# Performance work log

Measured on AMD Instinct MI355X. Metric: run time of the kernel, lower is better.

## Reference

```python
import jax, jax.numpy as jnp
import numpy as np

N_PTS = 32768      # n_x == n_y (query points == source points)
K_NBR = 32         # neighbors per query point
N_EDGES = N_PTS * K_NBR
D_COORD = 3
C = 64             # f_y channels == MLP output channels
H = 256            # MLP hidden width


def setup_inputs() -> dict:
    key = jax.random.key(0)
    ks = jax.random.split(key, 12)
    y = jax.random.normal(ks[0], (N_PTS, D_COORD), dtype=jnp.float32)
    x = jax.random.normal(ks[1], (N_PTS, D_COORD), dtype=jnp.float32)
    f_y = jax.random.normal(ks[2], (N_PTS, C), dtype=jnp.float32)
    neighbors_index = jax.random.randint(ks[3], (N_EDGES,), 0, N_PTS, dtype=jnp.int64)
    neighbors_row_splits = (jnp.arange(N_PTS + 1, dtype=jnp.int64) * K_NBR)
    weights = jax.random.uniform(ks[4], (N_EDGES,), dtype=jnp.float32)
    # LinearChannelMLP params: layers [6, 256, 256, 64], gelu between layers
    def dense(k, fan_in, fan_out):
        w = jax.random.normal(k, (fan_in, fan_out), dtype=jnp.float32) / np.sqrt(fan_in)
        return w
    W0 = dense(ks[5], 2 * D_COORD, H)
    b0 = jnp.zeros((H,), dtype=jnp.float32)
    W1 = dense(ks[6], H, H)
    b1 = jnp.zeros((H,), dtype=jnp.float32)
    W2 = dense(ks[7], H, C)
    b2 = jnp.zeros((C,), dtype=jnp.float32)
    return {"y": y, "x": x, "f_y": f_y,
            "neighbors_index": neighbors_index,
            "neighbors_row_splits": neighbors_row_splits,
            "weights": weights,
            "W0": W0, "b0": b0, "W1": W1, "b1": b1, "W2": W2, "b2": b2}


def reference(y, x, f_y, neighbors_index, neighbors_row_splits, weights,
              W0, b0, W1, b1, W2, b2):
    n_x = neighbors_row_splits.shape[0] - 1
    n_edges = neighbors_index.shape[0]
    # CSR row id for each edge (equivalent to repeat(arange(n_x), num_reps))
    seg = jnp.searchsorted(neighbors_row_splits, jnp.arange(n_edges), side='right') - 1
    rep_features = y[neighbors_index]            # [E, 3] gathered source coords
    self_features = x[seg]                       # [E, 3] repeated query coords
    agg = jnp.concatenate([rep_features, self_features], axis=-1)  # [E, 6]
    # channel MLP (gelu between layers, none after last)
    h = jax.nn.gelu(agg @ W0 + b0)
    h = jax.nn.gelu(h @ W1 + b1)
    rep = h @ W2 + b2                            # [E, C] kernel values
    # transform_type='linear': kernel * f_y(neighbor)
    rep = rep * f_y[neighbors_index]
    # quadrature weights (forces sum reduction, as in source)
    rep = rep * weights[:, None]
    out = jax.ops.segment_sum(rep, seg, num_segments=n_x)  # segment-CSR sum
    return out
```

## Files before the change

kernel.cpp:

```cpp
#include <hip/hip_runtime.h>
#include <hip/hip_bf16.h>
#include <stdint.h>

#define NPTS 32768
#define KNBR 32
#define NEDGES (NPTS * KNBR)
#define TM 128
#define AGG_STRIDE 40
#define H_STRIDE 264

typedef __attribute__((ext_vector_type(8))) short short8;
typedef __attribute__((ext_vector_type(4))) float f32x4;
typedef __attribute__((ext_vector_type(4))) unsigned int u32x4;

__device__ __forceinline__ unsigned short f2bf(float f) {
    unsigned int u = __float_as_uint(f);
    unsigned int r = (u + 0x7FFFu + ((u >> 16) & 1u)) >> 16;
    return (unsigned short)r;
}

__device__ __forceinline__ float gelu_tanh(float x) {
    float x2 = x * x;
    float inner = x * fmaf(0.044715f, x2, 1.0f);
    float e = __builtin_amdgcn_exp2f(-2.30220824f * inner);
    return x * __builtin_amdgcn_rcpf(1.0f + e);
}

__global__ void pack_w(const float* __restrict__ W0, const float* __restrict__ W1,
                       const float* __restrict__ W2, unsigned short* __restrict__ wp) {
    int tid = blockIdx.x * blockDim.x + threadIdx.x;
    if (tid >= 11264) return;
    unsigned short v[8];
    int l = tid & 63;
    if (tid < 1024) {
        int nt = tid >> 6;
        int n = nt * 16 + (l & 15);
        int k0 = (l >> 4) << 3;
        #pragma unroll
        for (int j = 0; j < 8; ++j) {
            int k = k0 + j;
            v[j] = f2bf(k < 6 ? W0[k * 256 + n] : 0.0f);
        }
    } else if (tid < 9216) {
        int q = tid - 1024;
        int nt = (q >> 6) & 15;
        int s = q >> 10;
        int n = nt * 16 + (l & 15);
        int k0 = s * 32 + ((l >> 4) << 3);
        #pragma unroll
        for (int j = 0; j < 8; ++j) v[j] = f2bf(W1[(k0 + j) * 256 + n]);
    } else {
        int q = tid - 9216;
        int nt = (q >> 6) & 3;
        int s = q >> 8;
        int n = nt * 16 + (l & 15);
        int k0 = s * 32 + ((l >> 4) << 3);
        #pragma unroll
        for (int j = 0; j < 8; ++j) v[j] = f2bf(W2[(k0 + j) * 64 + n]);
    }
    unsigned short* o = &wp[tid * 8];
    #pragma unroll
    for (int j = 0; j < 8; ++j) o[j] = v[j];
}

__global__ __launch_bounds__(256, 2)
void gno_fused(const float* __restrict__ y, const float* __restrict__ x,
               const float* __restrict__ f_y, const int* __restrict__ nbr,
               const float* __restrict__ wts,
               const float* __restrict__ b0, const float* __restrict__ b1,
               const float* __restrict__ b2,
               const unsigned short* __restrict__ wp,
               float* __restrict__ out) {
    __shared__ unsigned short agg_lds[TM * AGG_STRIDE];
    __shared__ unsigned short h_lds[TM * H_STRIDE];

    const int b = blockIdx.x;
    const int tid = threadIdx.x;
    const int l = tid & 63;
    const int w = tid >> 6;
    const int lg = l >> 4;
    const int ln = l & 15;
    const int ebase = b * TM;

    if (tid < TM) {
        int e = ebase + tid;
        int j = nbr[e];
        int i = e >> 5;
        float a0 = y[j * 3 + 0], a1 = y[j * 3 + 1], a2 = y[j * 3 + 2];
        float a3 = x[i * 3 + 0], a4 = x[i * 3 + 1], a5 = x[i * 3 + 2];
        unsigned int p0 = (unsigned int)f2bf(a0) | ((unsigned int)f2bf(a1) << 16);
        unsigned int p1 = (unsigned int)f2bf(a2) | ((unsigned int)f2bf(a3) << 16);
        unsigned int p2 = (unsigned int)f2bf(a4) | ((unsigned int)f2bf(a5) << 16);
        u32x4 q0 = {p0, p1, p2, 0u};
        u32x4 z  = {0u, 0u, 0u, 0u};
        unsigned short* row = &agg_lds[tid * AGG_STRIDE];
        *(u32x4*)(row +  0) = q0;
        *(u32x4*)(row +  8) = z;
        *(u32x4*)(row + 16) = z;
        *(u32x4*)(row + 24) = z;
    }
    __syncthreads();

    {
        short8 bw[4];
        float b0v[4];
        #pragma unroll
        for (int n = 0; n < 4; ++n) {
            int nt = 4 * w + n;
            bw[n] = *(const short8*)&wp[(nt * 64 + l) * 8];
            b0v[n] = b0[nt * 16 + ln];
        }
        f32x4 zero = {0.f, 0.f, 0.f, 0.f};
        #pragma unroll
        for (int mt = 0; mt < 8; ++mt) {
            short8 a = *(const short8*)&agg_lds[(mt * 16 + ln) * AGG_STRIDE + lg * 8];
            #pragma unroll
            for (int n = 0; n < 4; ++n) {
                f32x4 c = __builtin_amdgcn_mfma_f32_16x16x32_bf16(a, bw[n], zero, 0, 0, 0);
                int col = (4 * w + n) * 16 + ln;
                #pragma unroll
                for (int i = 0; i < 4; ++i) {
                    float g = gelu_tanh(c[i] + b0v[n]);
                    h_lds[(mt * 16 + lg * 4 + i) * H_STRIDE + col] = f2bf(g);
                }
            }
        }
    }
    __syncthreads();

    f32x4 acc[8][4];
    #pragma unroll
    for (int mt = 0; mt < 8; ++mt)
        #pragma unroll
        for (int n = 0; n < 4; ++n)
            acc[mt][n] = (f32x4){0.f, 0.f, 0.f, 0.f};

    for (int s = 0; s < 8; ++s) {
        short8 bw[4];
        #pragma unroll
        for (int n = 0; n < 4; ++n)
            bw[n] = *(const short8*)&wp[(1024 + (s * 16 + 4 * w + n) * 64 + l) * 8];
        #pragma unroll
        for (int mt = 0; mt < 8; ++mt) {
            short8 a = *(const short8*)&h_lds[(mt * 16 + ln) * H_STRIDE + s * 32 + lg * 8];
            #pragma unroll
            for (int n = 0; n < 4; ++n)
                acc[mt][n] = __builtin_amdgcn_mfma_f32_16x16x32_bf16(a, bw[n], acc[mt][n], 0, 0, 0);
        }
    }
    __syncthreads();

    {
        float b1v[4];
        #pragma unroll
        for (int n = 0; n < 4; ++n) b1v[n] = b1[(4 * w + n) * 16 + ln];
        #pragma unroll
        for (int mt = 0; mt < 8; ++mt) {
            #pragma unroll
            for (int n = 0; n < 4; ++n) {
                int col = (4 * w + n) * 16 + ln;
                #pragma unroll
                for (int i = 0; i < 4; ++i) {
                    float g = gelu_tanh(acc[mt][n][i] + b1v[n]);
                    h_lds[(mt * 16 + lg * 4 + i) * H_STRIDE + col] = f2bf(g);
                }
            }
        }
    }
    __syncthreads();

    f32x4 acc3[8];
    #pragma unroll
    for (int mt = 0; mt < 8; ++mt) acc3[mt] = (f32x4){0.f, 0.f, 0.f, 0.f};

    for (int s = 0; s < 8; ++s) {
        short8 bw = *(const short8*)&wp[(9216 + (s * 4 + w) * 64 + l) * 8];
        #pragma unroll
        for (int mt = 0; mt < 8; ++mt) {
            short8 a = *(const short8*)&h_lds[(mt * 16 + ln) * H_STRIDE + s * 32 + lg * 8];
            acc3[mt] = __builtin_amdgcn_mfma_f32_16x16x32_bf16(a, bw, acc3[mt], 0, 0, 0);
        }
    }

    {
        int col = w * 16 + ln;
        float b2v = b2[col];
        float p[4] = {0.f, 0.f, 0.f, 0.f};
        #pragma unroll
        for (int mt = 0; mt < 8; ++mt) {
            #pragma unroll
            for (int i = 0; i < 4; ++i) {
                int el = mt * 16 + lg * 4 + i;
                int e = ebase + el;
                int j = nbr[e];
                float v = acc3[mt][i] + b2v;
                v *= f_y[j * 64 + col] * wts[e];
                p[mt >> 1] += v;
            }
        }
        #pragma unroll
        for (int g = 0; g < 4; ++g) {
            float v = p[g];
            v += __shfl_xor(v, 16, 64);
            v += __shfl_xor(v, 32, 64);
            if (lg == 0) out[(b * 4 + g) * 64 + col] = v;
        }
    }
}

extern "C" void kernel_launch(void* const* d_in, const int* in_sizes, int n_in,
                              void* d_out, int out_size, void* d_ws, size_t ws_size,
                              hipStream_t stream) {
    const float* y   = (const float*)d_in[0];
    const float* x   = (const float*)d_in[1];
    const float* f_y = (const float*)d_in[2];
    const int*   nbr = (const int*)d_in[3];
    const float* wts = (const float*)d_in[5];
    const float* W0  = (const float*)d_in[6];
    const float* b0  = (const float*)d_in[7];
    const float* W1  = (const float*)d_in[8];
    const float* b1  = (const float*)d_in[9];
    const float* W2  = (const float*)d_in[10];
    const float* b2  = (const float*)d_in[11];
    unsigned short* wp = (unsigned short*)d_ws;
    float* out = (float*)d_out;

    pack_w<<<dim3(44), dim3(256), 0, stream>>>(W0, W1, W2, wp);
    gno_fused<<<dim3(NEDGES / TM), dim3(256), 0, stream>>>(
        y, x, f_y, nbr, wts, b0, b1, b2, wp, out);
}
```

Baseline: 304.4 us.

## Transpose MFMA operands, halve edge tile, vectorize LDS stores and epilogue

Swaps the MFMA operand order so weights act as A and activations as B. Each lane then holds four consecutive hidden columns for one edge, which allows packed 8-byte LDS stores of GELU outputs and vectorized bias and f_y loads in the epilogue. The edge tile shrinks from 128 to 64 and launch bounds are raised to 4 blocks per CU, aiming at higher occupancy with fewer accumulator registers. In exchange the segment reduction now needs four xor-shuffle rounds per component, and weights are reloaded from global memory for twice as many blocks.

```diff
diff --git a/kernel.cpp b/kernel.cpp
--- a/kernel.cpp
+++ b/kernel.cpp
@@ -5,13 +5,14 @@
 #define NPTS 32768
 #define KNBR 32
 #define NEDGES (NPTS * KNBR)
-#define TM 128
+#define TM 64
 #define AGG_STRIDE 40
 #define H_STRIDE 264
 
 typedef __attribute__((ext_vector_type(8))) short short8;
 typedef __attribute__((ext_vector_type(4))) float f32x4;
 typedef __attribute__((ext_vector_type(4))) unsigned int u32x4;
+typedef __attribute__((ext_vector_type(2))) unsigned int u32x2;
 
 __device__ __forceinline__ unsigned short f2bf(float f) {
     unsigned int u = __float_as_uint(f);
@@ -19,10 +20,21 @@
     return (unsigned short)r;
 }
 
+__device__ __forceinline__ unsigned int pack2bf(float a, float b) {
+    return (unsigned int)f2bf(a) | ((unsigned int)f2bf(b) << 16);
+}
+
+__device__ __forceinline__ void store_h4(unsigned short* p, float a, float b, float c, float d) {
+    u32x2 v;
+    v.x = pack2bf(a, b);
+    v.y = pack2bf(c, d);
+    *reinterpret_cast<u32x2*>(p) = v;
+}
+
 __device__ __forceinline__ float gelu_tanh(float x) {
     float x2 = x * x;
-    float inner = x * fmaf(0.044715f, x2, 1.0f);
-    float e = __builtin_amdgcn_exp2f(-2.30220824f * inner);
+    float u = fmaf(-0.102942496f, x2, -2.30220824f);
+    float e = __builtin_amdgcn_exp2f(x * u);
     return x * __builtin_amdgcn_rcpf(1.0f + e);
 }
 
@@ -63,7 +75,7 @@
     for (int j = 0; j < 8; ++j) o[j] = v[j];
 }
 
-__global__ __launch_bounds__(256, 2)
+__global__ __launch_bounds__(256, 4)
 void gno_fused(const float* __restrict__ y, const float* __restrict__ x,
                const float* __restrict__ f_y, const int* __restrict__ nbr,
                const float* __restrict__ wts,
@@ -71,8 +83,8 @@
                const float* __restrict__ b2,
                const unsigned short* __restrict__ wp,
                float* __restrict__ out) {
-    __shared__ unsigned short agg_lds[TM * AGG_STRIDE];
-    __shared__ unsigned short h_lds[TM * H_STRIDE];
+    __shared__ __align__(16) unsigned short agg_lds[TM * AGG_STRIDE];
+    __shared__ __align__(16) unsigned short h_lds[TM * H_STRIDE];
 
     const int b = blockIdx.x;
     const int tid = threadIdx.x;
@@ -86,13 +98,14 @@
         int e = ebase + tid;
         int j = nbr[e];
         int i = e >> 5;
-        float a0 = y[j * 3 + 0], a1 = y[j * 3 + 1], a2 = y[j * 3 + 2];
-        float a3 = x[i * 3 + 0], a4 = x[i * 3 + 1], a5 = x[i * 3 + 2];
-        unsigned int p0 = (unsigned int)f2bf(a0) | ((unsigned int)f2bf(a1) << 16);
-        unsigned int p1 = (unsigned int)f2bf(a2) | ((unsigned int)f2bf(a3) << 16);
-        unsigned int p2 = (unsigned int)f2bf(a4) | ((unsigned int)f2bf(a5) << 16);
-        u32x4 q0 = {p0, p1, p2, 0u};
-        u32x4 z  = {0u, 0u, 0u, 0u};
+        const float* yr = &y[j * 3];
+        const float* xr = &x[i * 3];
+        u32x4 q0;
+        q0.x = pack2bf(yr[0], yr[1]);
+        q0.y = pack2bf(yr[2], xr[0]);
+        q0.z = pack2bf(xr[1], xr[2]);
+        q0.w = 0u;
+        u32x4 z = {0u, 0u, 0u, 0u};
         unsigned short* row = &agg_lds[tid * AGG_STRIDE];
         *(u32x4*)(row +  0) = q0;
         *(u32x4*)(row +  8) = z;
@@ -102,108 +115,116 @@
     __syncthreads();
 
     {
-        short8 bw[4];
-        float b0v[4];
+        short8 aw[4];
+        f32x4 b0v[4];
         #pragma unroll
         for (int n = 0; n < 4; ++n) {
             int nt = 4 * w + n;
-            bw[n] = *(const short8*)&wp[(nt * 64 + l) * 8];
-            b0v[n] = b0[nt * 16 + ln];
+            aw[n] = *(const short8*)&wp[(nt * 64 + l) * 8];
+            b0v[n] = *(const f32x4*)&b0[nt * 16 + lg * 4];
         }
         f32x4 zero = {0.f, 0.f, 0.f, 0.f};
         #pragma unroll
-        for (int mt = 0; mt < 8; ++mt) {
-            short8 a = *(const short8*)&agg_lds[(mt * 16 + ln) * AGG_STRIDE + lg * 8];
+        for (int mt = 0; mt < 4; ++mt) {
+            short8 ag = *(const short8*)&agg_lds[(mt * 16 + ln) * AGG_STRIDE + lg * 8];
             #pragma unroll
             for (int n = 0; n < 4; ++n) {
-                f32x4 c = __builtin_amdgcn_mfma_f32_16x16x32_bf16(a, bw[n], zero, 0, 0, 0);
-                int col = (4 * w + n) * 16 + ln;
-                #pragma unroll
-                for (int i = 0; i < 4; ++i) {
-                    float g = gelu_tanh(c[i] + b0v[n]);
-                    h_lds[(mt * 16 + lg * 4 + i) * H_STRIDE + col] = f2bf(g);
-                }
+                f32x4 c = __builtin_amdgcn_mfma_f32_16x16x32_bf16(aw[n], ag, zero, 0, 0, 0);
+                float g0 = gelu_tanh(c[0] + b0v[n][0]);
+                float g1 = gelu_tanh(c[1] + b0v[n][1]);
+                float g2 = gelu_tanh(c[2] + b0v[n][2]);
+                float g3 = gelu_tanh(c[3] + b0v[n][3]);
+                store_h4(&h_lds[(mt * 16 + ln) * H_STRIDE + (4 * w + n) * 16 + lg * 4],
+                         g0, g1, g2, g3);
             }
         }
     }
     __syncthreads();
 
-    f32x4 acc[8][4];
-    #pragma unroll
-    for (int mt = 0; mt < 8; ++mt)
+    f32x4 acc[4][4];
+    #pragma unroll
+    for (int mt = 0; mt < 4; ++mt)
         #pragma unroll
         for (int n = 0; n < 4; ++n)
             acc[mt][n] = (f32x4){0.f, 0.f, 0.f, 0.f};
 
+    #pragma unroll
     for (int s = 0; s < 8; ++s) {
-        short8 bw[4];
+        short8 aw[4];
         #pragma unroll
         for (int n = 0; n < 4; ++n)
-            bw[n] = *(const short8*)&wp[(1024 + (s * 16 + 4 * w + n) * 64 + l) * 8];
-        #pragma unroll
-        for (int mt = 0; mt < 8; ++mt) {
-            short8 a = *(const short8*)&h_lds[(mt * 16 + ln) * H_STRIDE + s * 32 + lg * 8];
+            aw[n] = *(const short8*)&wp[(1024 + (s * 16 + 4 * w + n) * 64 + l) * 8];
+        #pragma unroll
+        for (int mt = 0; mt < 4; ++mt) {
+            short8 hb = *(const short8*)&h_lds[(mt * 16 + ln) * H_STRIDE + s * 32 + lg * 8];
             #pragma unroll
             for (int n = 0; n < 4; ++n)
-                acc[mt][n] = __builtin_amdgcn_mfma_f32_16x16x32_bf16(a, bw[n], acc[mt][n], 0, 0, 0);
+                acc[mt][n] = __builtin_amdgcn_mfma_f32_16x16x32_bf16(aw[n], hb, acc[mt][n], 0, 0, 0);
         }
     }
     __syncthreads();
 
     {
-        float b1v[4];
-        #pragma unroll
-        for (int n = 0; n < 4; ++n) b1v[n] = b1[(4 * w + n) * 16 + ln];
-        #pragma unroll
-        for (int mt = 0; mt < 8; ++mt) {
+        f32x4 b1v[4];
+        #pragma unroll
+        for (int n = 0; n < 4; ++n) b1v[n] = *(const f32x4*)&b1[(4 * w + n) * 16 + lg * 4];
+        #pragma unroll
+        for (int mt = 0; mt < 4; ++mt) {
             #pragma unroll
             for (int n = 0; n < 4; ++n) {
-                int col = (4 * w + n) * 16 + ln;
+                float g0 = gelu_tanh(acc[mt][n][0] + b1v[n][0]);
+                float g1 = gelu_tanh(acc[mt][n][1] + b1v[n][1]);
+                float g2 = gelu_tanh(acc[mt][n][2] + b1v[n][2]);
+                float g3 = gelu_tanh(acc[mt][n][3] + b1v[n][3]);
+                store_h4(&h_lds[(mt * 16 + ln) * H_STRIDE + (4 * w + n) * 16 + lg * 4],
+                         g0, g1, g2, g3);
+            }
+        }
+    }
+    __syncthreads();
+
+    f32x4 acc3[4];
+    #pragma unroll
+    for (int mt = 0; mt < 4; ++mt) acc3[mt] = (f32x4){0.f, 0.f, 0.f, 0.f};
+
+    #pragma unroll
+    for (int s = 0; s < 8; ++s) {
+        short8 aw = *(const short8*)&wp[(9216 + (s * 4 + w) * 64 + l) * 8];
+        #pragma unroll
+        for (int mt = 0; mt < 4; ++mt) {
+            short8 hb = *(const short8*)&h_lds[(mt * 16 + ln) * H_STRIDE + s * 32 + lg * 8];
+            acc3[mt] = __builtin_amdgcn_mfma_f32_16x16x32_bf16(aw, hb, acc3[mt], 0, 0, 0);
+        }
+    }
+
+    {
+        f32x4 b2v = *(const f32x4*)&b2[w * 16 + lg * 4];
+        f32x4 seg[2];
+        seg[0] = (f32x4){0.f, 0.f, 0.f, 0.f};
+        seg[1] = (f32x4){0.f, 0.f, 0.f, 0.f};
+        #pragma unroll
+        for (int mt = 0; mt < 4; ++mt) {
+            int e = ebase + mt * 16 + ln;
+            int j = nbr[e];
+            f32x4 fy = *(const f32x4*)&f_y[j * 64 + w * 16 + lg * 4];
+            float wt = wts[e];
+            f32x4 v;
+            #pragma unroll
+            for (int i = 0; i < 4; ++i)
+                v[i] = (acc3[mt][i] + b2v[i]) * fy[i] * wt;
+            seg[mt >> 1] += v;
+        }
+        #pragma unroll
+        for (int g = 0; g < 2; ++g) {
+            f32x4 v = seg[g];
+            #pragma unroll
+            for (int d = 1; d <= 8; d <<= 1) {
                 #pragma unroll
-                for (int i = 0; i < 4; ++i) {
-                    float g = gelu_tanh(acc[mt][n][i] + b1v[n]);
-                    h_lds[(mt * 16 + lg * 4 + i) * H_STRIDE + col] = f2bf(g);
-                }
+                for (int i = 0; i < 4; ++i)
+                    v[i] += __shfl_xor(v[i], d, 64);
             }
-        }
-    }
-    __syncthreads();
-
-    f32x4 acc3[8];
-    #pragma unroll
-    for (int mt = 0; mt < 8; ++mt) acc3[mt] = (f32x4){0.f, 0.f, 0.f, 0.f};
-
-    for (int s = 0; s < 8; ++s) {
-        short8 bw = *(const short8*)&wp[(9216 + (s * 4 + w) * 64 + l) * 8];
-        #pragma unroll
-        for (int mt = 0; mt < 8; ++mt) {
-            short8 a = *(const short8*)&h_lds[(mt * 16 + ln) * H_STRIDE + s * 32 + lg * 8];
-            acc3[mt] = __builtin_amdgcn_mfma_f32_16x16x32_bf16(a, bw, acc3[mt], 0, 0, 0);
-        }
-    }
-
-    {
-        int col = w * 16 + ln;
-        float b2v = b2[col];
-        float p[4] = {0.f, 0.f, 0.f, 0.f};
-        #pragma unroll
-        for (int mt = 0; mt < 8; ++mt) {
-            #pragma unroll
-            for (int i = 0; i < 4; ++i) {
-                int el = mt * 16 + lg * 4 + i;
-                int e = ebase + el;
-                int j = nbr[e];
-                float v = acc3[mt][i] + b2v;
-                v *= f_y[j * 64 + col] * wts[e];
-                p[mt >> 1] += v;
-            }
-        }
-        #pragma unroll
-        for (int g = 0; g < 4; ++g) {
-            float v = p[g];
-            v += __shfl_xor(v, 16, 64);
-            v += __shfl_xor(v, 32, 64);
-            if (lg == 0) out[(b * 4 + g) * 64 + col] = v;
+            if (ln == 0)
+                *(f32x4*)&out[(b * 2 + g) * 64 + w * 16 + lg * 4] = v;
         }
     }
 }
```

After: 298.0 us. 1.02x faster.
